# Kernel tuning notes

Measured on AMD Instinct MI355X. Metric: run time of the kernel, lower is better.

Reference implementation:

```python
import jax, jax.numpy as jnp
import numpy as np

B, L = 4096, 64          # batch, patch_len
OUT, KS, K = 64, 8, 4    # out_planes, kernel_size, num mixtures
STRIDE = 1
TEMP = 34.0
L_OUT = (L - KS) // STRIDE + 1   # 57
C = OUT * L_OUT                  # BN feature dim = 3648
HIDDEN = int(L * 0.5) + 1        # attention hidden planes = 33
EPS = 1e-5


def _gelu(x):
    return jax.nn.gelu(x, approximate=False)  # torch nn.GELU default = exact erf


def setup_inputs() -> dict:
    key = jax.random.key(0)
    ks = jax.random.split(key, 8)
    return {
        "x": jax.random.normal(ks[0], (B, L), jnp.float32),
        "fc1_w": jax.random.normal(ks[1], (HIDDEN, L), jnp.float32) * (2.0 / HIDDEN) ** 0.5,
        "fc2_w": jax.random.normal(ks[2], (K, HIDDEN), jnp.float32) * (2.0 / K) ** 0.5,
        "fc2_b": jnp.zeros((K,), jnp.float32),
        "weight": jax.random.normal(ks[3], (K, OUT, KS), jnp.float32) * 0.1,
        "bias": jnp.zeros((K, OUT), jnp.float32),
        "bn_gamma": jnp.ones((C,), jnp.float32),
        "bn_beta": jnp.zeros((C,), jnp.float32),
    }


def reference(x, fc1_w, fc2_w, fc2_b, weight, bias, bn_gamma, bn_beta):
    # --- attention1d: 1x1 convs over the patch_len 'channel' dim == linears ---
    a = _gelu(x @ fc1_w.T)                 # [B, HIDDEN]
    logits = a @ fc2_w.T + fc2_b           # [B, K]
    attn = jax.nn.softmax(logits / TEMP, axis=1)

    # --- sliding windows (im2col), shared by both conv paths ---
    idx = jnp.arange(L_OUT)[:, None] * STRIDE + jnp.arange(KS)[None, :]
    frames = x[:, idx]                     # [B, L_OUT, KS]

    # --- kernel_wise: full conv with each of the K kernels ---
    kw = jnp.einsum('blc,koc->bolk', frames, weight) + bias.T[None, :, None, :]  # [B,OUT,L_OUT,K]
    kw = kw.reshape(B, C, K)

    # --- per-sample aggregated kernel + grouped (per-sample) conv ---
    agg_w = jnp.einsum('bk,koc->boc', attn, weight)      # [B, OUT, KS]
    agg_b = attn @ bias                                  # [B, OUT]
    out = jnp.einsum('blc,boc->bol', frames, agg_w) + agg_b[:, :, None]  # [B,OUT,L_OUT]
    out = out.reshape(B, C)

    # --- BN(GELU(.)) with batch statistics (training-mode BatchNorm1d) ---
    g = _gelu(out)
    m = g.mean(axis=0)
    v = g.var(axis=0)
    out = (g - m) * jax.lax.rsqrt(v + EPS) * bn_gamma + bn_beta

    g2 = _gelu(kw)                                        # [B, C, K]
    m2 = g2.mean(axis=(0, 2), keepdims=True)
    v2 = g2.var(axis=(0, 2), keepdims=True)
    kw = (g2 - m2) * jax.lax.rsqrt(v2 + EPS) * bn_gamma[None, :, None] + bn_beta[None, :, None]

    return out, attn, kw.transpose(0, 2, 1)              # [B,C], [B,K], [B,K,C]
```

## Files before the change

kernel.cpp:

```cpp
#include <hip/hip_runtime.h>
#include <cstddef>

#define B_     4096
#define L_     64
#define OUT_   64
#define KS_    8
#define KK_    4
#define LOUT_  57
#define C_     3648
#define HID_   33
#define TEMP_  34.0f
#define EPS_   1e-5f
#define NCH_   128
#define SROWS_ 32
#define NB2_   32
#define PLANE_ (SROWS_ * 17 + 2)

typedef float f32x2 __attribute__((ext_vector_type(2)));

__device__ __forceinline__ f32x2 pk_fma(f32x2 a, f32x2 b, f32x2 c) {
    return __builtin_elementwise_fma(a, b, c);
}

__device__ __forceinline__ float gelu_f(float x) {
    float e = exp2f(-2.3022083f * x * fmaf(0.044715f * x, x, 1.0f));
    return x * __builtin_amdgcn_rcpf(1.0f + e);
}

__device__ __forceinline__ f32x2 gelu2(f32x2 x) {
    const f32x2 one = {1.f, 1.f};
    const f32x2 ca  = {0.044715f, 0.044715f};
    const f32x2 cb  = {-2.3022083f, -2.3022083f};
    f32x2 t = pk_fma(x * ca, x, one);
    f32x2 u = x * t * cb;
    f32x2 e = {exp2f(u.x), exp2f(u.y)};
    f32x2 d = e + one;
    f32x2 r = {__builtin_amdgcn_rcpf(d.x), __builtin_amdgcn_rcpf(d.y)};
    return x * r;
}

__device__ __forceinline__ void stage_shifted_p(
    const float* __restrict__ x, int b0, int tid, float4* xs4, int plane)
{
    for (int idx = tid; idx < SROWS_ * 16; idx += 256) {
        int r = idx >> 4, t = idx & 15;
        const float4* xrow = (const float4*)(x + (size_t)(b0 + r) * L_);
        float4 a  = xrow[t];
        float4 bq = xrow[t < 15 ? t + 1 : 15];
        int base = r * 17 + t;
        xs4[base]             = a;
        xs4[plane + base]     = make_float4(a.y, a.z, a.w, bq.x);
        xs4[2 * plane + base] = make_float4(a.z, a.w, bq.x, bq.y);
        xs4[3 * plane + base] = make_float4(a.w, bq.x, bq.y, bq.z);
    }
}

__global__ __launch_bounds__(256) void attn_kernel(
    const float* __restrict__ x, const float* __restrict__ fc1_w,
    const float* __restrict__ fc2_w, const float* __restrict__ fc2_b,
    float* __restrict__ attn_out)
{
    int tid = threadIdx.x;
    int r = tid >> 2, j = tid & 3;
    int b = blockIdx.x * 64 + r;
    const float4* xr4 = (const float4*)(x + (size_t)b * L_);
    float lg0 = 0.f, lg1 = 0.f, lg2 = 0.f, lg3 = 0.f;
    for (int h = j; h < HID_; h += 4) {
        const float4* f4 = (const float4*)(fc1_w + (size_t)h * L_);
        float acc = 0.f;
        #pragma unroll
        for (int i = 0; i < 16; ++i) {
            float4 xv = xr4[i], wv = f4[i];
            acc = fmaf(xv.x, wv.x, acc); acc = fmaf(xv.y, wv.y, acc);
            acc = fmaf(xv.z, wv.z, acc); acc = fmaf(xv.w, wv.w, acc);
        }
        float a = gelu_f(acc);
        lg0 = fmaf(a, fc2_w[h],             lg0);
        lg1 = fmaf(a, fc2_w[HID_ + h],      lg1);
        lg2 = fmaf(a, fc2_w[2 * HID_ + h],  lg2);
        lg3 = fmaf(a, fc2_w[3 * HID_ + h],  lg3);
    }
    lg0 += __shfl_xor(lg0, 1, 4); lg0 += __shfl_xor(lg0, 2, 4);
    lg1 += __shfl_xor(lg1, 1, 4); lg1 += __shfl_xor(lg1, 2, 4);
    lg2 += __shfl_xor(lg2, 1, 4); lg2 += __shfl_xor(lg2, 2, 4);
    lg3 += __shfl_xor(lg3, 1, 4); lg3 += __shfl_xor(lg3, 2, 4);
    if (j == 0) {
        float z0 = (lg0 + fc2_b[0]) * (1.0f / TEMP_);
        float z1 = (lg1 + fc2_b[1]) * (1.0f / TEMP_);
        float z2 = (lg2 + fc2_b[2]) * (1.0f / TEMP_);
        float z3 = (lg3 + fc2_b[3]) * (1.0f / TEMP_);
        float mx = fmaxf(fmaxf(z0, z1), fmaxf(z2, z3));
        float e0 = __expf(z0 - mx), e1 = __expf(z1 - mx);
        float e2 = __expf(z2 - mx), e3 = __expf(z3 - mx);
        float inv = __builtin_amdgcn_rcpf(e0 + e1 + e2 + e3);
        ((float4*)attn_out)[b] = make_float4(e0*inv, e1*inv, e2*inv, e3*inv);
    }
}

__global__ __launch_bounds__(256) void stats_kernel(
    const float* __restrict__ x, const float* __restrict__ weight,
    const float* __restrict__ bias, const float* __restrict__ attn,
    float* __restrict__ P, int use_partial)
{
    int cb = blockIdx.x;
    int chunk = blockIdx.y;
    int tid = threadIdx.x;
    int c = cb * 256 + tid;
    bool act = c < C_;
    int o = act ? (c / LOUT_) : 0;
    int l = act ? (c - o * LOUT_) : 0;
    int q = l >> 2, s = l & 3;

    f32x2 wp[KK_][4];
    float bk[KK_];
    #pragma unroll
    for (int k = 0; k < KK_; ++k) {
        bk[k] = bias[k * OUT_ + o];
        const float* wk = weight + (size_t)(k * OUT_ + o) * KS_;
        #pragma unroll
        for (int j = 0; j < 4; ++j) wp[k][j] = f32x2{wk[2*j], wk[2*j+1]};
    }

    __shared__ float4 xs4[4 * PLANE_];
    __shared__ float at[SROWS_][KK_];

    int b0 = chunk * SROWS_;
    stage_shifted_p(x, b0, tid, xs4, PLANE_);
    if (tid < SROWS_ * KK_) ((float*)at)[tid] = attn[(size_t)b0 * KK_ + tid];
    __syncthreads();

    float s1 = 0.f, s2 = 0.f;
    f32x2 t1v = {0.f, 0.f}, t2v = {0.f, 0.f};
    if (act) {
        const float4* base = &xs4[s * PLANE_ + q];
        #pragma unroll 4
        for (int r = 0; r < SROWS_; ++r) {
            float4 A  = base[r * 17];
            float4 Bv = base[r * 17 + 1];
            f32x2 xp[4] = {{A.x, A.y}, {A.z, A.w}, {Bv.x, Bv.y}, {Bv.z, Bv.w}};
            float kv[KK_];
            #pragma unroll
            for (int k = 0; k < KK_; ++k) {
                f32x2 acc = {bk[k], 0.f};
                #pragma unroll
                for (int j = 0; j < 4; ++j) acc = pk_fma(xp[j], wp[k][j], acc);
                kv[k] = acc.x + acc.y;
            }
            float ov = at[r][0] * kv[0];
            ov = fmaf(at[r][1], kv[1], ov);
            ov = fmaf(at[r][2], kv[2], ov);
            ov = fmaf(at[r][3], kv[3], ov);
            float g = gelu_f(ov);
            s1 += g; s2 = fmaf(g, g, s2);
            f32x2 g01 = gelu2(f32x2{kv[0], kv[1]});
            f32x2 g23 = gelu2(f32x2{kv[2], kv[3]});
            t1v = t1v + g01 + g23;
            t2v = pk_fma(g01, g01, t2v);
            t2v = pk_fma(g23, g23, t2v);
        }
    }
    if (!act) return;
    float t1 = t1v.x + t1v.y, t2 = t2v.x + t2v.y;
    if (use_partial) {
        size_t base = (size_t)chunk * 4 * C_ + c;
        P[base]          = s1;
        P[base + C_]     = s2;
        P[base + 2 * C_] = t1;
        P[base + 3 * C_] = t2;
    } else {
        atomicAdd(&P[c], s1);
        atomicAdd(&P[C_ + c], s2);
        atomicAdd(&P[2 * C_ + c], t1);
        atomicAdd(&P[3 * C_ + c], t2);
    }
}

__global__ __launch_bounds__(256) void finalize_kernel(
    const float* __restrict__ P, const float* __restrict__ gamma,
    const float* __restrict__ beta, float* __restrict__ F, int use_partial)
{
    __shared__ float red[4][64];
    int t = threadIdx.x;
    int cl = t & 63;
    int s = t >> 6;
    int c = blockIdx.x * 64 + cl;
    float a = 0.f;
    if (use_partial) {
        for (int ch = 0; ch < NCH_; ++ch)
            a += P[((size_t)ch * 4 + s) * C_ + c];
    } else {
        a = P[(size_t)s * C_ + c];
    }
    red[s][cl] = a;
    __syncthreads();
    if (t < 64) {
        float a0 = red[0][cl], a1 = red[1][cl], a2 = red[2][cl], a3 = red[3][cl];
        float m  = a0 * (1.0f / B_);
        float v  = a1 * (1.0f / B_) - m * m;
        float rs = rsqrtf(v + EPS_);
        float m2 = a2 * (1.0f / (B_ * KK_));
        float v2 = a3 * (1.0f / (B_ * KK_)) - m2 * m2;
        float rs2 = rsqrtf(v2 + EPS_);
        float ga = gamma[c], be = beta[c];
        F[c]          = rs * ga;
        F[C_ + c]     = be - m * rs * ga;
        F[2 * C_ + c] = rs2 * ga;
        F[3 * C_ + c] = be - m2 * rs2 * ga;
    }
}

__global__ __launch_bounds__(256) void write_kernel(
    const float* __restrict__ x, const float* __restrict__ weight,
    const float* __restrict__ bias, const float* __restrict__ attn,
    const float* __restrict__ F,
    float* __restrict__ out0, float* __restrict__ kwout)
{
    int cc = blockIdx.x;
    int bg = blockIdx.y;
    int tid = threadIdx.x;
    int c = cc * 256 + tid;
    bool act = c < C_;
    int o = act ? (c / LOUT_) : 0;
    int l = act ? (c - o * LOUT_) : 0;
    int q = l >> 2, s = l & 3;

    f32x2 wp[KK_][4];
    float bk[KK_];
    #pragma unroll
    for (int k = 0; k < KK_; ++k) {
        bk[k] = bias[k * OUT_ + o];
        const float* wk = weight + (size_t)(k * OUT_ + o) * KS_;
        #pragma unroll
        for (int j = 0; j < 4; ++j) wp[k][j] = f32x2{wk[2*j], wk[2*j+1]};
    }
    float sA = 0.f, hA = 0.f, sK = 0.f, hK = 0.f;
    if (act) {
        sA = F[c]; hA = F[C_ + c]; sK = F[2 * C_ + c]; hK = F[3 * C_ + c];
    }
    f32x2 sk2 = {sK, sK}, hk2 = {hK, hK};

    __shared__ float4 xs4[4 * PLANE_];
    __shared__ float at[NB2_][KK_];
    int b0 = bg * NB2_;
    stage_shifted_p(x, b0, tid, xs4, PLANE_);
    if (tid < NB2_ * KK_) ((float*)at)[tid] = attn[(size_t)b0 * KK_ + tid];
    __syncthreads();

    if (!act) return;

    const float4* xbase = &xs4[s * PLANE_ + q];
    #pragma unroll 4
    for (int r = 0; r < NB2_; ++r) {
        float4 A  = xbase[r * 17];
        float4 Bv = xbase[r * 17 + 1];
        f32x2 xp[4] = {{A.x, A.y}, {A.z, A.w}, {Bv.x, Bv.y}, {Bv.z, Bv.w}};
        float kv[KK_];
        #pragma unroll
        for (int k = 0; k < KK_; ++k) {
            f32x2 acc = {bk[k], 0.f};
            #pragma unroll
            for (int j = 0; j < 4; ++j) acc = pk_fma(xp[j], wp[k][j], acc);
            kv[k] = acc.x + acc.y;
        }
        float ov = at[r][0] * kv[0];
        ov = fmaf(at[r][1], kv[1], ov);
        ov = fmaf(at[r][2], kv[2], ov);
        ov = fmaf(at[r][3], kv[3], ov);
        int b = b0 + r;
        float g = gelu_f(ov);
        out0[(size_t)b * C_ + c] = fmaf(g, sA, hA);
        f32x2 g01 = gelu2(f32x2{kv[0], kv[1]});
        f32x2 g23 = gelu2(f32x2{kv[2], kv[3]});
        f32x2 r01 = pk_fma(g01, sk2, hk2);
        f32x2 r23 = pk_fma(g23, sk2, hk2);
        float* base = kwout + (size_t)b * KK_ * C_ + c;
        base[0]      = r01.x;
        base[C_]     = r01.y;
        base[2 * C_] = r23.x;
        base[3 * C_] = r23.y;
    }
}

extern "C" void kernel_launch(void* const* d_in, const int* in_sizes, int n_in,
                              void* d_out, int out_size, void* d_ws, size_t ws_size,
                              hipStream_t stream) {
    const float* x      = (const float*)d_in[0];
    const float* fc1_w  = (const float*)d_in[1];
    const float* fc2_w  = (const float*)d_in[2];
    const float* fc2_b  = (const float*)d_in[3];
    const float* weight = (const float*)d_in[4];
    const float* bias   = (const float*)d_in[5];
    const float* gamma  = (const float*)d_in[6];
    const float* beta   = (const float*)d_in[7];

    float* out  = (float*)d_out;
    float* out0 = out;
    float* attn = out + (size_t)B_ * C_;
    float* kwout = attn + (size_t)B_ * KK_;

    size_t need = (size_t)(NCH_ * 4 + 4) * C_ * sizeof(float);
    int use_partial = ws_size >= need;
    float* P = (float*)d_ws;
    float* F = P + (use_partial ? (size_t)NCH_ * 4 * C_ : (size_t)4 * C_);
    if (!use_partial)
        hipMemsetAsync(P, 0, 4 * C_ * sizeof(float), stream);

    attn_kernel<<<B_ / 64, 256, 0, stream>>>(x, fc1_w, fc2_w, fc2_b, attn);
    stats_kernel<<<dim3((C_ + 255) / 256, NCH_), 256, 0, stream>>>(
        x, weight, bias, attn, P, use_partial);
    finalize_kernel<<<C_ / 64, 256, 0, stream>>>(P, gamma, beta, F, use_partial);
    write_kernel<<<dim3((C_ + 255) / 256, B_ / NB2_), 256, 0, stream>>>(
        x, weight, bias, attn, F, out0, kwout);
}
```

Before: 143.0 us.

## Register-block stats kernel over four adjacent outputs per thread

The stats kernel now gives each thread a tile of four consecutive output positions of one channel. The 8 weights per mixture are held in registers and an unshifted x row is reused for all four outputs, so the four shifted LDS planes are no longer needed. The batch chunk drops from 32 to 16 rows and the chunk count doubles to 256, which keeps the grid wide. The cost is more partial-sum traffic, a larger finalize reduction, higher register pressure, and a tail tile with a single valid output.

Result: slower. 151.7 us (+6.1%).

```diff
diff --git a/kernel.cpp b/kernel.cpp
--- a/kernel.cpp
+++ b/kernel.cpp
@@ -11,12 +11,15 @@
 #define HID_   33
 #define TEMP_  34.0f
 #define EPS_   1e-5f
-#define NCH_   128
-#define SROWS_ 32
+#define NCH_   256
+#define SROWS_ 16
+#define XSTR_  68
+#define NTILE_ 960
 #define NB2_   32
-#define PLANE_ (SROWS_ * 17 + 2)
+#define PLANE_ (NB2_ * 17 + 2)
 
 typedef float f32x2 __attribute__((ext_vector_type(2)));
+typedef float f32x4 __attribute__((ext_vector_type(4)));
 
 __device__ __forceinline__ f32x2 pk_fma(f32x2 a, f32x2 b, f32x2 c) {
     return __builtin_elementwise_fma(a, b, c);
@@ -37,22 +40,6 @@
     f32x2 d = e + one;
     f32x2 r = {__builtin_amdgcn_rcpf(d.x), __builtin_amdgcn_rcpf(d.y)};
     return x * r;
-}
-
-__device__ __forceinline__ void stage_shifted_p(
-    const float* __restrict__ x, int b0, int tid, float4* xs4, int plane)
-{
-    for (int idx = tid; idx < SROWS_ * 16; idx += 256) {
-        int r = idx >> 4, t = idx & 15;
-        const float4* xrow = (const float4*)(x + (size_t)(b0 + r) * L_);
-        float4 a  = xrow[t];
-        float4 bq = xrow[t < 15 ? t + 1 : 15];
-        int base = r * 17 + t;
-        xs4[base]             = a;
-        xs4[plane + base]     = make_float4(a.y, a.z, a.w, bq.x);
-        xs4[2 * plane + base] = make_float4(a.z, a.w, bq.x, bq.y);
-        xs4[3 * plane + base] = make_float4(a.w, bq.x, bq.y, bq.z);
-    }
 }
 
 __global__ __launch_bounds__(256) void attn_kernel(
@@ -102,76 +89,103 @@
     const float* __restrict__ bias, const float* __restrict__ attn,
     float* __restrict__ P, int use_partial)
 {
-    int cb = blockIdx.x;
+    int tid = threadIdx.x;
+    int tile = blockIdx.x * 256 + tid;
     int chunk = blockIdx.y;
-    int tid = threadIdx.x;
-    int c = cb * 256 + tid;
-    bool act = c < C_;
-    int o = act ? (c / LOUT_) : 0;
-    int l = act ? (c - o * LOUT_) : 0;
-    int q = l >> 2, s = l & 3;
-
-    f32x2 wp[KK_][4];
+    bool act = tile < NTILE_;
+    int o  = act ? tile / 15 : 0;
+    int lt = act ? tile - o * 15 : 0;
+    int l0 = lt * 4;
+    int c0 = o * LOUT_ + l0;
+    int nvalid = (lt == 14) ? 1 : 4;
+
+    float w[KK_][KS_];
     float bk[KK_];
     #pragma unroll
     for (int k = 0; k < KK_; ++k) {
         bk[k] = bias[k * OUT_ + o];
-        const float* wk = weight + (size_t)(k * OUT_ + o) * KS_;
         #pragma unroll
-        for (int j = 0; j < 4; ++j) wp[k][j] = f32x2{wk[2*j], wk[2*j+1]};
-    }
-
-    __shared__ float4 xs4[4 * PLANE_];
-    __shared__ float at[SROWS_][KK_];
-
+        for (int t = 0; t < KS_; ++t) w[k][t] = weight[(k * OUT_ + o) * KS_ + t];
+    }
+
+    __shared__ float xs[SROWS_ * XSTR_];
+    __shared__ float4 at4[SROWS_];
     int b0 = chunk * SROWS_;
-    stage_shifted_p(x, b0, tid, xs4, PLANE_);
-    if (tid < SROWS_ * KK_) ((float*)at)[tid] = attn[(size_t)b0 * KK_ + tid];
+    for (int idx = tid; idx < SROWS_ * 17; idx += 256) {
+        int r = idx / 17, t = idx - r * 17;
+        const float4* xrow = (const float4*)(x + (size_t)(b0 + r) * L_);
+        *(float4*)&xs[r * XSTR_ + 4 * t] = xrow[t < 16 ? t : 15];
+    }
+    if (tid < SROWS_) at4[tid] = *(const float4*)(attn + (size_t)(b0 + tid) * KK_);
     __syncthreads();
 
-    float s1 = 0.f, s2 = 0.f;
-    f32x2 t1v = {0.f, 0.f}, t2v = {0.f, 0.f};
+    f32x4 s1 = {0,0,0,0}, s2 = {0,0,0,0}, t1 = {0,0,0,0}, t2 = {0,0,0,0};
     if (act) {
-        const float4* base = &xs4[s * PLANE_ + q];
-        #pragma unroll 4
+        const float* xr = &xs[l0];
+        #pragma unroll 2
         for (int r = 0; r < SROWS_; ++r) {
-            float4 A  = base[r * 17];
-            float4 Bv = base[r * 17 + 1];
-            f32x2 xp[4] = {{A.x, A.y}, {A.z, A.w}, {Bv.x, Bv.y}, {Bv.z, Bv.w}};
-            float kv[KK_];
+            const float* p = xr + r * XSTR_;
+            float4 X0 = *(const float4*)p;
+            float4 X1 = *(const float4*)(p + 4);
+            float4 X2 = *(const float4*)(p + 8);
+            float xw[12] = {X0.x,X0.y,X0.z,X0.w, X1.x,X1.y,X1.z,X1.w,
+                            X2.x,X2.y,X2.z,X2.w};
+            float4 atv = at4[r];
+            float kv[4][KK_];
             #pragma unroll
             for (int k = 0; k < KK_; ++k) {
-                f32x2 acc = {bk[k], 0.f};
+                f32x2 aA = {bk[k], bk[k]}, aB = {bk[k], bk[k]};
                 #pragma unroll
-                for (int j = 0; j < 4; ++j) acc = pk_fma(xp[j], wp[k][j], acc);
-                kv[k] = acc.x + acc.y;
+                for (int t = 0; t < KS_; ++t) {
+                    f32x2 ws = {w[k][t], w[k][t]};
+                    aA = pk_fma(f32x2{xw[t],     xw[t + 1]}, ws, aA);
+                    aB = pk_fma(f32x2{xw[t + 2], xw[t + 3]}, ws, aB);
+                }
+                kv[0][k] = aA.x; kv[1][k] = aA.y; kv[2][k] = aB.x; kv[3][k] = aB.y;
             }
-            float ov = at[r][0] * kv[0];
-            ov = fmaf(at[r][1], kv[1], ov);
-            ov = fmaf(at[r][2], kv[2], ov);
-            ov = fmaf(at[r][3], kv[3], ov);
-            float g = gelu_f(ov);
-            s1 += g; s2 = fmaf(g, g, s2);
-            f32x2 g01 = gelu2(f32x2{kv[0], kv[1]});
-            f32x2 g23 = gelu2(f32x2{kv[2], kv[3]});
-            t1v = t1v + g01 + g23;
-            t2v = pk_fma(g01, g01, t2v);
-            t2v = pk_fma(g23, g23, t2v);
+            f32x4 g4;
+            #pragma unroll
+            for (int e = 0; e < 4; ++e) {
+                float ov = atv.x * kv[e][0];
+                ov = fmaf(atv.y, kv[e][1], ov);
+                ov = fmaf(atv.z, kv[e][2], ov);
+                ov = fmaf(atv.w, kv[e][3], ov);
+                g4[e] = gelu_f(ov);
+            }
+            s1 = s1 + g4;
+            s2 = __builtin_elementwise_fma(g4, g4, s2);
+            #pragma unroll
+            for (int e = 0; e < 4; e += 2) {
+                #pragma unroll
+                for (int k = 0; k < KK_; k += 2) {
+                    f32x2 ga = gelu2(f32x2{kv[e][k],     kv[e][k + 1]});
+                    f32x2 gb = gelu2(f32x2{kv[e + 1][k], kv[e + 1][k + 1]});
+                    t1[e]     += ga.x + ga.y;
+                    t1[e + 1] += gb.x + gb.y;
+                    t2[e]     = fmaf(ga.x, ga.x, t2[e]);
+                    t2[e]     = fmaf(ga.y, ga.y, t2[e]);
+                    t2[e + 1] = fmaf(gb.x, gb.x, t2[e + 1]);
+                    t2[e + 1] = fmaf(gb.y, gb.y, t2[e + 1]);
+                }
+            }
         }
     }
     if (!act) return;
-    float t1 = t1v.x + t1v.y, t2 = t2v.x + t2v.y;
     if (use_partial) {
-        size_t base = (size_t)chunk * 4 * C_ + c;
-        P[base]          = s1;
-        P[base + C_]     = s2;
-        P[base + 2 * C_] = t1;
-        P[base + 3 * C_] = t2;
+        size_t base = (size_t)chunk * 4 * C_ + c0;
+        for (int e = 0; e < nvalid; ++e) {
+            P[base + e]          = s1[e];
+            P[base + C_ + e]     = s2[e];
+            P[base + 2 * C_ + e] = t1[e];
+            P[base + 3 * C_ + e] = t2[e];
+        }
     } else {
-        atomicAdd(&P[c], s1);
-        atomicAdd(&P[C_ + c], s2);
-        atomicAdd(&P[2 * C_ + c], t1);
-        atomicAdd(&P[3 * C_ + c], t2);
+        for (int e = 0; e < nvalid; ++e) {
+            atomicAdd(&P[c0 + e], s1[e]);
+            atomicAdd(&P[C_ + c0 + e], s2[e]);
+            atomicAdd(&P[2 * C_ + c0 + e], t1[e]);
+            atomicAdd(&P[3 * C_ + c0 + e], t2[e]);
+        }
     }
 }
 
@@ -206,6 +220,22 @@
         F[C_ + c]     = be - m * rs * ga;
         F[2 * C_ + c] = rs2 * ga;
         F[3 * C_ + c] = be - m2 * rs2 * ga;
+    }
+}
+
+__device__ __forceinline__ void stage_shifted_p(
+    const float* __restrict__ x, int b0, int tid, float4* xs4, int plane)
+{
+    for (int idx = tid; idx < NB2_ * 16; idx += 256) {
+        int r = idx >> 4, t = idx & 15;
+        const float4* xrow = (const float4*)(x + (size_t)(b0 + r) * L_);
+        float4 a  = xrow[t];
+        float4 bq = xrow[t < 15 ? t + 1 : 15];
+        int base = r * 17 + t;
+        xs4[base]             = a;
+        xs4[plane + base]     = make_float4(a.y, a.z, a.w, bq.x);
+        xs4[2 * plane + base] = make_float4(a.z, a.w, bq.x, bq.y);
+        xs4[3 * plane + base] = make_float4(a.w, bq.x, bq.y, bq.z);
     }
 }
 
@@ -306,7 +336,7 @@
         hipMemsetAsync(P, 0, 4 * C_ * sizeof(float), stream);
 
     attn_kernel<<<B_ / 64, 256, 0, stream>>>(x, fc1_w, fc2_w, fc2_b, attn);
-    stats_kernel<<<dim3((C_ + 255) / 256, NCH_), 256, 0, stream>>>(
+    stats_kernel<<<dim3(4, NCH_), 256, 0, stream>>>(
         x, weight, bias, attn, P, use_partial);
     finalize_kernel<<<C_ / 64, 256, 0, stream>>>(P, gamma, beta, F, use_partial);
     write_kernel<<<dim3((C_ + 255) / 256, B_ / NB2_), 256, 0, stream>>>(
```
